# Kernel tuning notes

Measured on AMD Instinct MI355X. Metric: run time of the kernel, lower is better.

Reference implementation:

```python
import jax, jax.numpy as jnp
import numpy as np

SIZE = (128.0, 128.0, 128.0)
FEATURE_BLOCK_IDS = (1, 2, 3)


def _trilerp(feat, coords, power):
    # feat: [B, D, H, W, C]; coords: [B, N, 3] in [0, 1]
    B = coords.shape[0]
    scale = jnp.asarray([0.5 ** power * SIZE[0],
                         0.5 ** power * SIZE[1],
                         0.5 ** power * SIZE[2]], dtype=coords.dtype)
    hi = float(min(feat.shape[1:4])) - 1.01
    idx = jnp.clip(coords * scale, 0.01, hi)  # [B, N, 3]
    ix, iy, iz = idx[..., 0], idx[..., 1], idx[..., 2]
    x1, x2 = jnp.floor(ix), jnp.ceil(ix)
    y1, y2 = jnp.floor(iy), jnp.ceil(iy)
    z1, z2 = jnp.floor(iz), jnp.ceil(iz)
    b = jnp.arange(B)[:, None]  # broadcast batch index

    def g(xi, yi, zi):
        return feat[b, xi.astype(jnp.int32), yi.astype(jnp.int32), zi.astype(jnp.int32)]

    wx, wx2 = (ix - x1)[..., None], (x2 - ix)[..., None]
    wy, wy2 = (iy - y1)[..., None], (y2 - iy)[..., None]
    wz, wz2 = (iz - z1)[..., None], (z2 - iz)[..., None]

    # z = z1 plane
    lerp_x1 = g(x2, y1, z1) * wx + g(x1, y1, z1) * wx2
    lerp_x2 = g(x2, y2, z1) * wx + g(x1, y2, z1) * wx2
    lerp_y1 = lerp_x2 * wy + lerp_x1 * wy2
    # z = z2 plane
    lerp_x1 = g(x2, y1, z2) * wx + g(x1, y1, z2) * wx2
    lerp_x2 = g(x2, y2, z2) * wx + g(x1, y2, z2) * wx2
    lerp_y2 = lerp_x2 * wy + lerp_x1 * wy2
    return lerp_y2 * wz + lerp_y1 * wz2  # [B, N, C]


def setup_inputs() -> dict:
    key = jax.random.key(0)
    ks = jax.random.split(key, 7)
    B, N = 2, 50000
    return {
        'features0': jax.random.normal(ks[0], (B, 128, 128, 128, 1), jnp.float32),
        'features1': jax.random.normal(ks[1], (B, 64, 64, 64, 32), jnp.float32),
        'features2': jax.random.normal(ks[2], (B, 32, 32, 32, 64), jnp.float32),
        'features3': jax.random.normal(ks[3], (B, 16, 16, 16, 128), jnp.float32),
        'features4': jax.random.normal(ks[4], (B, 8, 8, 8, 256), jnp.float32),
        'mesh_coords': jax.random.uniform(ks[5], (B, N, 3), jnp.float32),
        'mesh_features': jax.random.normal(ks[6], (B, N, 3), jnp.float32),
    }


def reference(features0, features1, features2, features3, features4, mesh_coords, mesh_features):
    feats = [features0, features1, features2, features3, features4]
    # mesh_coords is [B, N, 3] -> one coord group, reshape is identity
    sampled = [_trilerp(feats[i], mesh_coords, i) for i in FEATURE_BLOCK_IDS]
    out = jnp.concatenate(sampled, axis=-1)
    return jnp.concatenate([out, mesh_features], axis=-1)
```

## Files before the change

### kernel.cpp

```cpp
#include <hip/hip_runtime.h>


typedef float floatx4 __attribute__((ext_vector_type(4)));

__device__ __forceinline__ int point_batch(int p, int N) {
    int b = 0;
    while (p >= N) { p -= N; ++b; }
    return b;
}

__device__ __forceinline__ int bucket_of(const float* __restrict__ coords,
                                         int p, int N) {
    const float cx = coords[p * 3 + 0];
    const float cy = coords[p * 3 + 1];
    const float cz = coords[p * 3 + 2];
    int bx = (int)(cx * 16.0f); bx = bx < 0 ? 0 : (bx > 15 ? 15 : bx);
    int by = (int)(cy * 16.0f); by = by < 0 ? 0 : (by > 15 ? 15 : by);
    int bz = (int)(cz * 16.0f); bz = bz < 0 ? 0 : (bz > 15 ? 15 : bz);
    return ((point_batch(p, N) * 16 + bx) * 16 + by) * 16 + bz;
}

__global__ __launch_bounds__(256) void hist_kernel(
    const float* __restrict__ coords, unsigned* __restrict__ bins,
    int N, int P)
{
    const int p = blockIdx.x * 256 + (int)threadIdx.x;
    if (p < P) atomicAdd(&bins[bucket_of(coords, p, N)], 1u);
}

__global__ __launch_bounds__(1024) void scan_kernel(unsigned* __restrict__ bins)
{
    __shared__ unsigned part[1024];
    const int t = threadIdx.x;
    unsigned loc[8];
    unsigned s = 0;
    for (int i = 0; i < 8; ++i) {
        unsigned v = bins[t * 8 + i];
        loc[i] = s;
        s += v;
    }
    part[t] = s;
    __syncthreads();
    for (int off = 1; off < 1024; off <<= 1) {
        unsigned v = (t >= off) ? part[t - off] : 0u;
        __syncthreads();
        part[t] += v;
        __syncthreads();
    }
    const unsigned base = (t == 0) ? 0u : part[t - 1];
    for (int i = 0; i < 8; ++i) bins[t * 8 + i] = base + loc[i];
}

__global__ __launch_bounds__(256) void scatter_kernel(
    const float* __restrict__ coords, unsigned* __restrict__ bins,
    unsigned* __restrict__ perm, int N, int P)
{
    const int p = blockIdx.x * 256 + (int)threadIdx.x;
    if (p < P) {
        const unsigned pos = atomicAdd(&bins[bucket_of(coords, p, N)], 1u);
        perm[pos] = (unsigned)p;
    }
}

template<int D, int LPP, int OCB>
__device__ __forceinline__ void do_level(const float* __restrict__ fbase,
                                         const float* __restrict__ coords,
                                         const unsigned* __restrict__ perm,
                                         float* __restrict__ out,
                                         int sBase, int N, int P)
{
    const int tid  = threadIdx.x;
    const int lane = tid & 63;
    const int wv   = tid >> 6;
    const int slot = sBase + wv * (64 / LPP) + (lane / LPP);
    const int c4   = lane & (LPP - 1);
    if (slot >= P) return;
    const int p = perm ? (int)perm[slot] : slot;

    const float cx = coords[p * 3 + 0];
    const float cy = coords[p * 3 + 1];
    const float cz = coords[p * 3 + 2];

    const float scale = (float)D;
    const float hi    = (float)((double)D - 1.01);

    const float ix = fminf(fmaxf(cx * scale, 0.01f), hi);
    const float iy = fminf(fmaxf(cy * scale, 0.01f), hi);
    const float iz = fminf(fmaxf(cz * scale, 0.01f), hi);

    const float x1f = floorf(ix), x2f = ceilf(ix);
    const float y1f = floorf(iy), y2f = ceilf(iy);
    const float z1f = floorf(iz), z2f = ceilf(iz);
    const int x1 = (int)x1f, x2 = (int)x2f;
    const int y1 = (int)y1f, y2 = (int)y2f;
    const int z1 = (int)z1f, z2 = (int)z2f;

    const float wx = ix - x1f, wx2 = x2f - ix;
    const float wy = iy - y1f, wy2 = y2f - iy;
    const float wz = iz - z1f, wz2 = z2f - iz;

    const unsigned baseB = (unsigned)point_batch(p, N) * (unsigned)(D * D * D * LPP * 16)
                         + (unsigned)c4 * 16u;
    #define OFFB(X, Y, Z) (baseB + (unsigned)((((X) * D + (Y)) * D + (Z)) * LPP) * 16u)

    floatx4 v111, v211, v121, v221, v112, v212, v122, v222;
    asm volatile("global_load_dwordx4 %0, %1, %2"
                 : "=v"(v111) : "v"(OFFB(x1, y1, z1)), "s"(fbase));
    asm volatile("global_load_dwordx4 %0, %1, %2"
                 : "=v"(v211) : "v"(OFFB(x2, y1, z1)), "s"(fbase));
    asm volatile("global_load_dwordx4 %0, %1, %2"
                 : "=v"(v121) : "v"(OFFB(x1, y2, z1)), "s"(fbase));
    asm volatile("global_load_dwordx4 %0, %1, %2"
                 : "=v"(v221) : "v"(OFFB(x2, y2, z1)), "s"(fbase));
    asm volatile("global_load_dwordx4 %0, %1, %2"
                 : "=v"(v112) : "v"(OFFB(x1, y1, z2)), "s"(fbase));
    asm volatile("global_load_dwordx4 %0, %1, %2"
                 : "=v"(v212) : "v"(OFFB(x2, y1, z2)), "s"(fbase));
    asm volatile("global_load_dwordx4 %0, %1, %2"
                 : "=v"(v122) : "v"(OFFB(x1, y2, z2)), "s"(fbase));
    asm volatile("global_load_dwordx4 %0, %1, %2"
                 : "=v"(v222) : "v"(OFFB(x2, y2, z2)), "s"(fbase));
    #undef OFFB

    asm volatile("s_waitcnt vmcnt(0)");
    __builtin_amdgcn_sched_barrier(0);

    const floatx4 lx1a = v211 * wx + v111 * wx2;
    const floatx4 lx2a = v221 * wx + v121 * wx2;
    const floatx4 ly1  = lx2a * wy + lx1a * wy2;
    const floatx4 lx1b = v212 * wx + v112 * wx2;
    const floatx4 lx2b = v222 * wx + v122 * wx2;
    const floatx4 ly2  = lx2b * wy + lx1b * wy2;
    const floatx4 r    = ly2  * wz + ly1  * wz2;

    float* o = out + p * 227 + OCB + c4 * 4;
    __builtin_nontemporal_store(r.x, o + 0);
    __builtin_nontemporal_store(r.y, o + 1);
    __builtin_nontemporal_store(r.z, o + 2);
    __builtin_nontemporal_store(r.w, o + 3);
}

__global__ __launch_bounds__(256, 8) void trilerp_kernel(
    const float* __restrict__ f1,
    const float* __restrict__ f2,
    const float* __restrict__ f3,
    const float* __restrict__ coords,
    const float* __restrict__ meshf,
    const unsigned* __restrict__ perm,
    float* __restrict__ out,
    int N, int P, int nb1, int nb2, int nb3)
{
    const int nwg  = (int)gridDim.x;
    const int orig = (int)blockIdx.x;
    const int q = nwg >> 3, r = nwg & 7;
    const int xcd = orig & 7, j = orig >> 3;
    const int blk = (xcd < r ? xcd * (q + 1) : r * (q + 1) + (xcd - r) * q) + j;

    if (blk < nb1) {
        do_level<64, 8, 0>(f1, coords, perm, out, blk * 32, N, P);
    } else if (blk < nb1 + nb2) {
        do_level<32, 16, 32>(f2, coords, perm, out, (blk - nb1) * 16, N, P);
    } else if (blk < nb1 + nb2 + nb3) {
        do_level<16, 32, 96>(f3, coords, perm, out, (blk - nb1 - nb2) * 8, N, P);
    } else {
        const int e = (blk - nb1 - nb2 - nb3) * 256 + (int)threadIdx.x;
        if (e < P * 3) {
            const int p = e / 3, c = e - p * 3;
            __builtin_nontemporal_store(meshf[e], &out[p * 227 + 224 + c]);
        }
    }
}

extern "C" void kernel_launch(void* const* d_in, const int* in_sizes, int n_in,
                              void* d_out, int out_size, void* d_ws, size_t ws_size,
                              hipStream_t stream) {
    const float* f1     = (const float*)d_in[1];
    const float* f2     = (const float*)d_in[2];
    const float* f3     = (const float*)d_in[3];
    const float* coords = (const float*)d_in[5];
    const float* meshf  = (const float*)d_in[6];
    float* out = (float*)d_out;

    const int B = in_sizes[1] / (64 * 64 * 64 * 32);
    const int N = in_sizes[5] / (B * 3);
    const int P = B * N;

    const int NBINS = 8192;
    const size_t ws_need = (size_t)NBINS * 4 + (size_t)P * 4;
    unsigned* bins = (unsigned*)d_ws;
    unsigned* perm = bins + NBINS;
    const bool do_sort = (d_ws != nullptr) && (ws_size >= ws_need);

    if (do_sort) {
        hipMemsetAsync(bins, 0, NBINS * 4, stream);
        const int nbp = (P + 255) / 256;
        hist_kernel<<<dim3(nbp), dim3(256), 0, stream>>>(coords, bins, N, P);
        scan_kernel<<<dim3(1), dim3(1024), 0, stream>>>(bins);
        scatter_kernel<<<dim3(nbp), dim3(256), 0, stream>>>(coords, bins, perm, N, P);
    }

    const int nb1 = (P + 31) / 32;
    const int nb2 = (P + 15) / 16;
    const int nb3 = (P + 7) / 8;
    const int nbm = (P * 3 + 255) / 256;
    const int grid = nb1 + nb2 + nb3 + nbm;

    trilerp_kernel<<<dim3(grid), dim3(256), 0, stream>>>(
        f1, f2, f3, coords, meshf, do_sort ? perm : nullptr,
        out, N, P, nb1, nb2, nb3);
}
```

Before: 255.9 us.

## Scatter sorted coordinates and swizzle block indices per level segment

```diff
diff --git a/kernel.cpp b/kernel.cpp
--- a/kernel.cpp
+++ b/kernel.cpp
@@ -53,18 +53,29 @@
 
 __global__ __launch_bounds__(256) void scatter_kernel(
     const float* __restrict__ coords, unsigned* __restrict__ bins,
-    unsigned* __restrict__ perm, int N, int P)
+    unsigned* __restrict__ perm, float* __restrict__ csort,
+    int N, int P)
 {
     const int p = blockIdx.x * 256 + (int)threadIdx.x;
     if (p < P) {
         const unsigned pos = atomicAdd(&bins[bucket_of(coords, p, N)], 1u);
         perm[pos] = (unsigned)p;
-    }
+        csort[pos * 3 + 0] = coords[p * 3 + 0];
+        csort[pos * 3 + 1] = coords[p * 3 + 1];
+        csort[pos * 3 + 2] = coords[p * 3 + 2];
+    }
+}
+
+__device__ __forceinline__ int seg_swz(int lo, int S) {
+    const int q = S >> 3, r = S & 7;
+    const int xcd = lo & 7, j = lo >> 3;
+    return (xcd < r ? xcd * (q + 1) : r * (q + 1) + (xcd - r) * q) + j;
 }
 
 template<int D, int LPP, int OCB>
 __device__ __forceinline__ void do_level(const float* __restrict__ fbase,
                                          const float* __restrict__ coords,
+                                         const float* __restrict__ csort,
                                          const unsigned* __restrict__ perm,
                                          float* __restrict__ out,
                                          int sBase, int N, int P)
@@ -77,9 +88,10 @@
     if (slot >= P) return;
     const int p = perm ? (int)perm[slot] : slot;
 
-    const float cx = coords[p * 3 + 0];
-    const float cy = coords[p * 3 + 1];
-    const float cz = coords[p * 3 + 2];
+    const float* cp = csort ? (csort + slot * 3) : (coords + p * 3);
+    const float cx = cp[0];
+    const float cy = cp[1];
+    const float cz = cp[2];
 
     const float scale = (float)D;
     const float hi    = (float)((double)D - 1.01);
@@ -146,24 +158,23 @@
     const float* __restrict__ f3,
     const float* __restrict__ coords,
     const float* __restrict__ meshf,
+    const float* __restrict__ csort,
     const unsigned* __restrict__ perm,
     float* __restrict__ out,
     int N, int P, int nb1, int nb2, int nb3)
 {
-    const int nwg  = (int)gridDim.x;
     const int orig = (int)blockIdx.x;
-    const int q = nwg >> 3, r = nwg & 7;
-    const int xcd = orig & 7, j = orig >> 3;
-    const int blk = (xcd < r ? xcd * (q + 1) : r * (q + 1) + (xcd - r) * q) + j;
-
-    if (blk < nb1) {
-        do_level<64, 8, 0>(f1, coords, perm, out, blk * 32, N, P);
-    } else if (blk < nb1 + nb2) {
-        do_level<32, 16, 32>(f2, coords, perm, out, (blk - nb1) * 16, N, P);
-    } else if (blk < nb1 + nb2 + nb3) {
-        do_level<16, 32, 96>(f3, coords, perm, out, (blk - nb1 - nb2) * 8, N, P);
+    if (orig < nb1) {
+        const int blk = seg_swz(orig, nb1);
+        do_level<64, 8, 0>(f1, coords, csort, perm, out, blk * 32, N, P);
+    } else if (orig < nb1 + nb2) {
+        const int blk = seg_swz(orig - nb1, nb2);
+        do_level<32, 16, 32>(f2, coords, csort, perm, out, blk * 16, N, P);
+    } else if (orig < nb1 + nb2 + nb3) {
+        const int blk = seg_swz(orig - nb1 - nb2, nb3);
+        do_level<16, 32, 96>(f3, coords, csort, perm, out, blk * 8, N, P);
     } else {
-        const int e = (blk - nb1 - nb2 - nb3) * 256 + (int)threadIdx.x;
+        const int e = (orig - nb1 - nb2 - nb3) * 256 + (int)threadIdx.x;
         if (e < P * 3) {
             const int p = e / 3, c = e - p * 3;
             __builtin_nontemporal_store(meshf[e], &out[p * 227 + 224 + c]);
@@ -186,9 +197,10 @@
     const int P = B * N;
 
     const int NBINS = 8192;
-    const size_t ws_need = (size_t)NBINS * 4 + (size_t)P * 4;
-    unsigned* bins = (unsigned*)d_ws;
-    unsigned* perm = bins + NBINS;
+    const size_t ws_need = (size_t)NBINS * 4 + (size_t)P * 4 + (size_t)P * 12;
+    unsigned* bins  = (unsigned*)d_ws;
+    unsigned* perm  = bins + NBINS;
+    float*    csort = (float*)(perm + P);
     const bool do_sort = (d_ws != nullptr) && (ws_size >= ws_need);
 
     if (do_sort) {
@@ -196,7 +208,8 @@
         const int nbp = (P + 255) / 256;
         hist_kernel<<<dim3(nbp), dim3(256), 0, stream>>>(coords, bins, N, P);
         scan_kernel<<<dim3(1), dim3(1024), 0, stream>>>(bins);
-        scatter_kernel<<<dim3(nbp), dim3(256), 0, stream>>>(coords, bins, perm, N, P);
+        scatter_kernel<<<dim3(nbp), dim3(256), 0, stream>>>(coords, bins, perm,
+                                                            csort, N, P);
     }
 
     const int nb1 = (P + 31) / 32;
@@ -206,6 +219,7 @@
     const int grid = nb1 + nb2 + nb3 + nbm;
 
     trilerp_kernel<<<dim3(grid), dim3(256), 0, stream>>>(
-        f1, f2, f3, coords, meshf, do_sort ? perm : nullptr,
+        f1, f2, f3, coords, meshf,
+        do_sort ? csort : nullptr, do_sort ? perm : nullptr,
         out, N, P, nb1, nb2, nb3);
 }
```

New measurement: 232.8 us. 1.1x faster.
